# Performance work log

Hardware: AMD Instinct MI355X
Metric: run time of the kernel (lower is better)

## Reference

```python
import jax, jax.numpy as jnp
import numpy as np

D = 768
H = 12
HD = D // H
EPS = 1e-5

def layer_norm(x, g, b):
    xf = x.astype(jnp.float32)
    mu = jnp.mean(xf, axis=-1, keepdims=True)
    var = jnp.var(xf, axis=-1, keepdims=True)
    return ((xf - mu) * jax.lax.rsqrt(var + EPS) * g + b).astype(x.dtype)

def quick_gelu(x):
    return x * jax.nn.sigmoid(1.702 * x)

def setup_inputs() -> dict:
    key = jax.random.key(0)
    ks = jax.random.split(key, 8)
    L, N = 257, 64
    s = 1.0 / np.sqrt(D)
    return {
        "x": jax.random.normal(ks[0], (L, N, D), dtype=jnp.float32),
        "in_proj_w": jax.random.normal(ks[1], (3 * D, D), dtype=jnp.float32) * s,
        "in_proj_b": jnp.zeros((3 * D,), dtype=jnp.float32),
        "out_proj_w": jax.random.normal(ks[2], (D, D), dtype=jnp.float32) * s,
        "out_proj_b": jnp.zeros((D,), dtype=jnp.float32),
        "ln1_g": jnp.ones((D,), dtype=jnp.float32),
        "ln1_b": jnp.zeros((D,), dtype=jnp.float32),
        "ln2_g": jnp.ones((D,), dtype=jnp.float32),
        "ln2_b": jnp.zeros((D,), dtype=jnp.float32),
        "fc_w": jax.random.normal(ks[3], (D, D), dtype=jnp.float32) * s,
        "fc_b": jnp.zeros((D,), dtype=jnp.float32),
    }

def reference(x, in_proj_w, in_proj_b, out_proj_w, out_proj_b,
              ln1_g, ln1_b, ln2_g, ln2_b, fc_w, fc_b):
    L, N, _ = x.shape
    h = layer_norm(x, ln1_g, ln1_b)                      # [L,N,D]
    qkv = h @ in_proj_w.T + in_proj_b                    # [L,N,3D]
    q, k, v = jnp.split(qkv, 3, axis=-1)
    q = q.reshape(L, N, H, HD)
    k = k.reshape(L, N, H, HD)
    v = v.reshape(L, N, H, HD)
    scale = 1.0 / np.sqrt(HD)
    scores = jnp.einsum('lnhd,mnhd->nhlm', q, k) * scale  # [N,H,L,L]
    weights = jax.nn.softmax(scores, axis=-1)             # per-head attn weights
    attn = jnp.einsum('nhlm,mnhd->lnhd', weights, v).reshape(L, N, D)
    attn_out = attn @ out_proj_w.T + out_proj_b
    x = x + attn_out
    h2 = layer_norm(x, ln2_g, ln2_b)
    x = x + quick_gelu(h2 @ fc_w.T + fc_b)
    return x, weights
```

## Files before the change

kernel.cpp:

```cpp
#include <hip/hip_runtime.h>
#include <cstdint>

#define D_MODEL 768
#define NHEAD 12
#define HDIM 64
#define LSEQ 257
#define NBATCH 64
#define MROWS (LSEQ*NBATCH)

typedef unsigned short u16;
typedef __attribute__((ext_vector_type(8))) short short8;
typedef __attribute__((ext_vector_type(4))) float floatx4;

__device__ __forceinline__ float b2f(u16 u){ return __uint_as_float(((unsigned)u)<<16); }
__device__ __forceinline__ u16 f2bf(float f){
  unsigned x = __float_as_uint(f);
  return (u16)((x + 0x7fffu + ((x>>16)&1u)) >> 16);
}

__device__ __forceinline__ void async16(const u16* g, u16* l) {
  __builtin_amdgcn_global_load_lds(
      (const __attribute__((address_space(1))) unsigned int*)g,
      (__attribute__((address_space(3))) unsigned int*)l, 16, 0, 0);
}

__global__ __launch_bounds__(256) void cvt_bf16(const float* __restrict__ in,
                                                u16* __restrict__ out, int n8)
{
  int i = blockIdx.x*256 + threadIdx.x;
  if (i >= n8) return;
  const float4* p = (const float4*)in + (size_t)i*2;
  float4 a = p[0], b = p[1];
  u16 t[8] = {f2bf(a.x),f2bf(a.y),f2bf(a.z),f2bf(a.w),
              f2bf(b.x),f2bf(b.y),f2bf(b.z),f2bf(b.w)};
  *(uint4*)(out + (size_t)i*8) = *(const uint4*)t;
}

template<typename TIN>
__global__ __launch_bounds__(256) void ln_kernel(const TIN* __restrict__ x,
    const float* __restrict__ g, const float* __restrict__ b,
    u16* __restrict__ out, int rows)
{
  int wv = threadIdx.x >> 6, lane = threadIdx.x & 63;
  int row = blockIdx.x*4 + wv;
  if (row >= rows) return;
  const TIN* xr = x + (size_t)row*D_MODEL;
  float v[12]; float s = 0.f, s2 = 0.f;
#pragma unroll
  for (int i=0;i<12;++i){
    float f;
    if constexpr (sizeof(TIN)==2) f = b2f(((const u16*)xr)[lane + i*64]);
    else                          f = ((const float*)xr)[lane + i*64];
    v[i]=f; s+=f; s2+=f*f;
  }
#pragma unroll
  for (int o=32;o>0;o>>=1){ s += __shfl_xor(s,o,64); s2 += __shfl_xor(s2,o,64); }
  float mu = s*(1.f/768.f);
  float var = fmaxf(s2*(1.f/768.f) - mu*mu, 0.f);
  float rs = rsqrtf(var + 1e-5f);
  u16* orow = out + (size_t)row*D_MODEL;
#pragma unroll
  for (int i=0;i<12;++i){
    int c = lane + i*64;
    orow[c] = f2bf((v[i]-mu)*rs*g[c] + b[c]);
  }
}

#define BM 128
#define BN 128
#define BK 32

template<int EPI>
__global__ __launch_bounds__(256,2) void gemm_bt(
    const u16* __restrict__ A, const u16* __restrict__ B,
    const float* __restrict__ bias, void* __restrict__ Cout,
    const void* __restrict__ resid, int M, int N, int K)
{
  __shared__ u16 sA[BM*BK];
  __shared__ u16 sB[BN*BK];
  const int m0 = blockIdx.y * BM, n0 = blockIdx.x * BN;
  const int tid = threadIdx.x;
  const int lane = tid & 63, w = tid >> 6;
  const int wm = (w>>1)*64, wn = (w&1)*64;
  const int l16 = lane & 15, quad = lane >> 4;
  const int srow = lane >> 2, scol = (lane & 3)*8;
  int ar0 = m0 + w*32 + srow;      if (ar0 >= M) ar0 = M-1;
  int ar1 = m0 + w*32 + 16 + srow; if (ar1 >= M) ar1 = M-1;
  const u16* gA0 = A + (size_t)ar0*K + scol;
  const u16* gA1 = A + (size_t)ar1*K + scol;
  const u16* gB  = B + (size_t)(n0 + w*32 + srow)*K + scol;
  u16* lA0 = sA + w*32*BK;
  u16* lB0 = sB + w*32*BK;

  floatx4 acc[4][4];
#pragma unroll
  for (int i=0;i<4;++i)
#pragma unroll
    for (int j=0;j<4;++j) acc[i][j] = (floatx4){0.f,0.f,0.f,0.f};

  for (int k0=0;k0<K;k0+=BK) {
    async16(gA0 + k0,       lA0);
    async16(gA1 + k0,       lA0 + 16*BK);
    async16(gB  + k0,       lB0);
    async16(gB  + k0 + 16*K, lB0 + 16*BK);
    __syncthreads();
    short8 af[4], bfr[4];
#pragma unroll
    for (int t=0;t<4;++t) af[t]  = *(const short8*)(sA + (wm + t*16 + l16)*BK + quad*8);
#pragma unroll
    for (int t=0;t<4;++t) bfr[t] = *(const short8*)(sB + (wn + t*16 + l16)*BK + quad*8);
#pragma unroll
    for (int mt=0;mt<4;++mt)
#pragma unroll
      for (int nt=0;nt<4;++nt)
        acc[mt][nt] = __builtin_amdgcn_mfma_f32_16x16x32_bf16(af[mt], bfr[nt], acc[mt][nt], 0,0,0);
    __syncthreads();
  }

#pragma unroll
  for (int mt=0;mt<4;++mt)
#pragma unroll
    for (int nt=0;nt<4;++nt) {
      int col = n0 + wn + nt*16 + l16;
      if (col >= N) continue;
      float bia = bias[col];
      int rowb = m0 + wm + mt*16 + quad*4;
#pragma unroll
      for (int r=0;r<4;++r) {
        int row = rowb + r;
        if (row >= M) continue;
        float vacc = acc[mt][nt][r] + bia;
        size_t off = (size_t)row*N + col;
        if (EPI==0) {
          ((u16*)Cout)[off] = f2bf(vacc);
        } else if (EPI==1) {
          ((u16*)Cout)[off] = f2bf(((const float*)resid)[off] + vacc);
        } else {
          float gl = vacc / (1.f + __expf(-1.702f*vacc));
          ((float*)Cout)[off] = b2f(((const u16*)resid)[off]) + gl;
        }
      }
    }
}

__global__ __launch_bounds__(256,2) void attn_kernel(
    const u16* __restrict__ qkv, float* __restrict__ wout, u16* __restrict__ attn)
{
  __shared__ __align__(16) u16 smem[29696];
  u16* sQ  = smem;
  u16* sK  = smem + 64*72;
  u16* sP  = smem;
  u16* sVt = smem + 64*296;
  const int p = blockIdx.x;
  const int n = p / NHEAD, h = p % NHEAD;
  const int l0 = blockIdx.y * 64;
  const int tid = threadIdx.x, lane = tid & 63, w = tid >> 6;
  const int l16 = lane & 15, quad = lane >> 4;

  for (int i = tid; i < 64*8; i += 256) {
    int lr = i >> 3, c8 = (i & 7)*8;
    uint4 v = {0u,0u,0u,0u};
    int gl = l0 + lr;
    if (gl < LSEQ) v = *(const uint4*)(qkv + ((size_t)gl*NBATCH + n)*2304 + h*HDIM + c8);
    *(uint4*)(sQ + lr*72 + c8) = v;
  }
  for (int i = tid; i < 272*8; i += 256) {
    int kr = i >> 3, c8 = (i & 7)*8;
    uint4 v = {0u,0u,0u,0u};
    if (kr < LSEQ) v = *(const uint4*)(qkv + ((size_t)kr*NBATCH + n)*2304 + 768 + h*HDIM + c8);
    *(uint4*)(sK + kr*72 + c8) = v;
  }
  __syncthreads();

  floatx4 acc[17];
#pragma unroll
  for (int t=0;t<17;++t) acc[t] = (floatx4){0.f,0.f,0.f,0.f};
#pragma unroll
  for (int ks=0;ks<2;++ks) {
    short8 aq = *(const short8*)(sQ + (w*16 + l16)*72 + ks*32 + quad*8);
#pragma unroll
    for (int nt=0;nt<17;++nt) {
      short8 bk = *(const short8*)(sK + (nt*16 + l16)*72 + ks*32 + quad*8);
      acc[nt] = __builtin_amdgcn_mfma_f32_16x16x32_bf16(aq, bk, acc[nt], 0,0,0);
    }
  }
  __syncthreads();

#pragma unroll
  for (int r=0;r<4;++r) {
    float mx = -3.0e38f;
#pragma unroll
    for (int nt=0;nt<17;++nt) {
      int col = nt*16 + l16;
      float v = (col < LSEQ) ? acc[nt][r]*0.125f : -3.0e38f;
      acc[nt][r] = v;
      mx = fmaxf(mx, v);
    }
#pragma unroll
    for (int o=1;o<16;o<<=1) mx = fmaxf(mx, __shfl_xor(mx,o,64));
    float sum = 0.f;
#pragma unroll
    for (int nt=0;nt<17;++nt) {
      float e = __expf(acc[nt][r]-mx);
      acc[nt][r] = e; sum += e;
    }
#pragma unroll
    for (int o=1;o<16;o<<=1) sum += __shfl_xor(sum,o,64);
    float inv = 1.f/sum;
#pragma unroll
    for (int nt=0;nt<17;++nt) acc[nt][r] *= inv;
  }

  size_t wbase = (size_t)p * LSEQ * LSEQ;
#pragma unroll
  for (int r=0;r<4;++r) {
    int lr = w*16 + quad*4 + r;
    int gl = l0 + lr;
#pragma unroll
    for (int nt=0;nt<17;++nt) {
      int col = nt*16 + l16;
      sP[lr*296 + col] = f2bf(acc[nt][r]);
      if (gl < LSEQ && col < LSEQ) wout[wbase + (size_t)gl*LSEQ + col] = acc[nt][r];
    }
  }
  for (int i = tid; i < 64*16; i += 256) {
    int lr = i >> 4, c = 272 + (i & 15);
    sP[lr*296 + c] = 0;
  }
  __syncthreads();

  floatx4 acc2[4];
#pragma unroll
  for (int t=0;t<4;++t) acc2[t] = (floatx4){0.f,0.f,0.f,0.f};
  for (int c=0;c<2;++c) {
    if (c) __syncthreads();
    int mbase = c*160;
    int msz = c ? 128 : 160;
    for (int ml = tid; ml < msz; ml += 256) {
      int m = mbase + ml;
      if (m < LSEQ) {
        const u16* vr = qkv + ((size_t)m*NBATCH + n)*2304 + 1536 + h*HDIM;
#pragma unroll
        for (int d=0; d<64; ++d) sVt[d*168 + ml] = vr[d];
      } else {
#pragma unroll
        for (int d=0; d<64; ++d) sVt[d*168 + ml] = 0;
      }
    }
    __syncthreads();
    int nks = c ? 4 : 5;
    for (int ksl=0; ksl<nks; ++ksl) {
      short8 ap = *(const short8*)(sP + (w*16 + l16)*296 + mbase + ksl*32 + quad*8);
#pragma unroll
      for (int nt=0;nt<4;++nt) {
        short8 bv = *(const short8*)(sVt + (nt*16 + l16)*168 + ksl*32 + quad*8);
        acc2[nt] = __builtin_amdgcn_mfma_f32_16x16x32_bf16(ap, bv, acc2[nt], 0,0,0);
      }
    }
  }
#pragma unroll
  for (int nt=0;nt<4;++nt)
#pragma unroll
    for (int r=0;r<4;++r) {
      int lr = w*16 + quad*4 + r;
      int gl = l0 + lr;
      if (gl < LSEQ) {
        int d = nt*16 + l16;
        attn[((size_t)gl*NBATCH + n)*768 + h*HDIM + d] = f2bf(acc2[nt][r]);
      }
    }
}

extern "C" void kernel_launch(void* const* d_in, const int* in_sizes, int n_in,
                              void* d_out, int out_size, void* d_ws, size_t ws_size,
                              hipStream_t stream)
{
  (void)in_sizes; (void)n_in; (void)out_size; (void)ws_size;
  const float* x    = (const float*)d_in[0];
  const float* w_in = (const float*)d_in[1];
  const float* b_in = (const float*)d_in[2];
  const float* w_op = (const float*)d_in[3];
  const float* b_op = (const float*)d_in[4];
  const float* g1   = (const float*)d_in[5];
  const float* b1   = (const float*)d_in[6];
  const float* g2   = (const float*)d_in[7];
  const float* b2v  = (const float*)d_in[8];
  const float* wfc  = (const float*)d_in[9];
  const float* bfc  = (const float*)d_in[10];

  float* out_x = (float*)d_out;
  float* out_w = out_x + (size_t)MROWS*D_MODEL;

  char* ws = (char*)d_ws;
  u16* qkv  = (u16*)ws;
  u16* hbuf = (u16*)(ws + (size_t)MROWS*2304*2);
  u16* x2b  = (u16*)(ws + (size_t)MROWS*2304*2 + (size_t)MROWS*768*2);

  u16* w_in_bf = x2b;
  u16* w_op_bf = qkv + (size_t)24*1024*1024;
  u16* w_fc_bf = w_op_bf + 768*768;

  dim3 blk(256);
  cvt_bf16<<<dim3(864), blk, 0, stream>>>(w_in, w_in_bf, 221184);
  ln_kernel<float><<<dim3(MROWS/4), blk, 0, stream>>>(x, g1, b1, hbuf, MROWS);
  gemm_bt<0><<<dim3(18,129), blk, 0, stream>>>(hbuf, w_in_bf, b_in, qkv, nullptr, MROWS, 2304, 768);
  attn_kernel<<<dim3(768,5), blk, 0, stream>>>(qkv, out_w, hbuf);
  cvt_bf16<<<dim3(288), blk, 0, stream>>>(w_op, w_op_bf, 73728);
  cvt_bf16<<<dim3(288), blk, 0, stream>>>(wfc,  w_fc_bf, 73728);
  gemm_bt<1><<<dim3(6,129), blk, 0, stream>>>(hbuf, w_op_bf, b_op, x2b, x, MROWS, 768, 768);
  ln_kernel<u16><<<dim3(MROWS/4), blk, 0, stream>>>(x2b, g2, b2v, qkv, MROWS);
  gemm_bt<2><<<dim3(6,129), blk, 0, stream>>>(qkv, w_fc_bf, bfc, out_x, x2b, MROWS, 768, 768);
}
```

Before: 643.2 us.

## Pre-transpose V into a separate buffer so attention loads it with vector reads

Adds a kernel that transposes each head's V slice into a [head][d][m] layout through swizzled shared memory, and stores it in the not-yet-written output buffer. The attention kernel then fills its transposed-V tile with 16-byte vector loads instead of scalar strided global reads and scalar LDS writes. This removes uncoalesced V traffic that is repeated by all five query-tile blocks per head, at the cost of an extra launch and an extra global round trip of V.

```diff
diff --git a/kernel.cpp b/kernel.cpp
--- a/kernel.cpp
+++ b/kernel.cpp
@@ -7,6 +7,7 @@
 #define LSEQ 257
 #define NBATCH 64
 #define MROWS (LSEQ*NBATCH)
+#define VSTRIDE 288
 
 typedef unsigned short u16;
 typedef __attribute__((ext_vector_type(8))) short short8;
@@ -34,6 +35,37 @@
   u16 t[8] = {f2bf(a.x),f2bf(a.y),f2bf(a.z),f2bf(a.w),
               f2bf(b.x),f2bf(b.y),f2bf(b.z),f2bf(b.w)};
   *(uint4*)(out + (size_t)i*8) = *(const uint4*)t;
+}
+
+__global__ __launch_bounds__(256) void vtr_kernel(const u16* __restrict__ qkv,
+                                                  u16* __restrict__ vT)
+{
+  __shared__ __align__(16) u16 t[64][72];
+  const int p = blockIdx.x, mc = blockIdx.y;
+  const int n = p / NHEAD, h = p % NHEAD;
+  const int m0 = mc*64;
+  const int tid = threadIdx.x;
+  for (int i = tid; i < 512; i += 256) {
+    int mr = i >> 3, c8 = (i & 7)*8;
+    uint4 v = {0u,0u,0u,0u};
+    int m = m0 + mr;
+    if (m < LSEQ) v = *(const uint4*)(qkv + ((size_t)m*NBATCH + n)*2304 + 1536 + h*HDIM + c8);
+    *(uint4*)(&t[mr][c8 ^ ((mr&7)<<3)]) = v;
+  }
+  __syncthreads();
+  for (int i = tid; i < 512; i += 256) {
+    int d  = (i >> 1) & 63;
+    int mo = (((i & 1) | ((i >> 7) << 1))) * 8;
+    int mg = m0 + mo;
+    if (mg >= VSTRIDE) continue;
+    u16 tmp[8];
+#pragma unroll
+    for (int j = 0; j < 8; ++j) {
+      int mr = mo + j;
+      tmp[j] = t[mr][((d & ~7) ^ ((mr & 7) << 3)) | (d & 7)];
+    }
+    *(uint4*)(vT + ((size_t)p*HDIM + d)*VSTRIDE + mg) = *(const uint4*)tmp;
+  }
 }
 
 template<typename TIN>
@@ -99,9 +131,9 @@
     for (int j=0;j<4;++j) acc[i][j] = (floatx4){0.f,0.f,0.f,0.f};
 
   for (int k0=0;k0<K;k0+=BK) {
-    async16(gA0 + k0,       lA0);
-    async16(gA1 + k0,       lA0 + 16*BK);
-    async16(gB  + k0,       lB0);
+    async16(gA0 + k0,        lA0);
+    async16(gA1 + k0,        lA0 + 16*BK);
+    async16(gB  + k0,        lB0);
     async16(gB  + k0 + 16*K, lB0 + 16*BK);
     __syncthreads();
     short8 af[4], bfr[4];
@@ -144,7 +176,8 @@
 }
 
 __global__ __launch_bounds__(256,2) void attn_kernel(
-    const u16* __restrict__ qkv, float* __restrict__ wout, u16* __restrict__ attn)
+    const u16* __restrict__ qkv, const u16* __restrict__ vT,
+    float* __restrict__ wout, u16* __restrict__ attn)
 {
   __shared__ __align__(16) u16 smem[29696];
   u16* sQ  = smem;
@@ -229,6 +262,7 @@
   }
   __syncthreads();
 
+  const u16* vTp = vT + (size_t)p*HDIM*VSTRIDE;
   floatx4 acc2[4];
 #pragma unroll
   for (int t=0;t<4;++t) acc2[t] = (floatx4){0.f,0.f,0.f,0.f};
@@ -236,16 +270,11 @@
     if (c) __syncthreads();
     int mbase = c*160;
     int msz = c ? 128 : 160;
-    for (int ml = tid; ml < msz; ml += 256) {
-      int m = mbase + ml;
-      if (m < LSEQ) {
-        const u16* vr = qkv + ((size_t)m*NBATCH + n)*2304 + 1536 + h*HDIM;
-#pragma unroll
-        for (int d=0; d<64; ++d) sVt[d*168 + ml] = vr[d];
-      } else {
-#pragma unroll
-        for (int d=0; d<64; ++d) sVt[d*168 + ml] = 0;
-      }
+    int nvec = msz >> 3;
+    for (int i = tid; i < 64*nvec; i += 256) {
+      int d = i / nvec, jm = (i - d*nvec)*8;
+      uint4 v = *(const uint4*)(vTp + (size_t)d*VSTRIDE + mbase + jm);
+      *(uint4*)(sVt + d*168 + jm) = v;
     }
     __syncthreads();
     int nks = c ? 4 : 5;
@@ -299,12 +328,14 @@
   u16* w_in_bf = x2b;
   u16* w_op_bf = qkv + (size_t)24*1024*1024;
   u16* w_fc_bf = w_op_bf + 768*768;
+  u16* vT = (u16*)out_x;
 
   dim3 blk(256);
   cvt_bf16<<<dim3(864), blk, 0, stream>>>(w_in, w_in_bf, 221184);
   ln_kernel<float><<<dim3(MROWS/4), blk, 0, stream>>>(x, g1, b1, hbuf, MROWS);
   gemm_bt<0><<<dim3(18,129), blk, 0, stream>>>(hbuf, w_in_bf, b_in, qkv, nullptr, MROWS, 2304, 768);
-  attn_kernel<<<dim3(768,5), blk, 0, stream>>>(qkv, out_w, hbuf);
+  vtr_kernel<<<dim3(768,5), blk, 0, stream>>>(qkv, vT);
+  attn_kernel<<<dim3(768,5), blk, 0, stream>>>(qkv, vT, out_w, hbuf);
   cvt_bf16<<<dim3(288), blk, 0, stream>>>(w_op, w_op_bf, 73728);
   cvt_bf16<<<dim3(288), blk, 0, stream>>>(wfc,  w_fc_bf, 73728);
   gemm_bt<1><<<dim3(6,129), blk, 0, stream>>>(hbuf, w_op_bf, b_op, x2b, x, MROWS, 768, 768);
```

Measured after the change: 665.2 us. +3.4%, slower.

## Double-buffer GEMM LDS tiles with XOR swizzle and remap attention grid

Applied to the files above, without the earlier changes.

The GEMM now double-buffers its A/B LDS tiles. The next K-tile is prefetched with global_load_lds while the current tile is consumed, using explicit vmcnt waits and raw barriers. An XOR swizzle on the 16-byte column chunks is meant to reduce LDS bank conflicts on the fragment reads. The attention launch is flattened to a 1D grid with a remap that interleaves blocks across 8 groups, likely targeting XCD locality so blocks sharing K/V land on the same die. LDS use doubles, which may affect occupancy.

```diff
diff --git a/kernel.cpp b/kernel.cpp
--- a/kernel.cpp
+++ b/kernel.cpp
@@ -76,21 +76,22 @@
     const float* __restrict__ bias, void* __restrict__ Cout,
     const void* __restrict__ resid, int M, int N, int K)
 {
-  __shared__ u16 sA[BM*BK];
-  __shared__ u16 sB[BN*BK];
+  __shared__ u16 sA[2][BM*BK];
+  __shared__ u16 sB[2][BN*BK];
   const int m0 = blockIdx.y * BM, n0 = blockIdx.x * BN;
   const int tid = threadIdx.x;
   const int lane = tid & 63, w = tid >> 6;
   const int wm = (w>>1)*64, wn = (w&1)*64;
   const int l16 = lane & 15, quad = lane >> 4;
-  const int srow = lane >> 2, scol = (lane & 3)*8;
+  const int srow = lane >> 2;
+  const int scol = ((lane & 3) ^ ((srow >> 1) & 3)) * 8;
   int ar0 = m0 + w*32 + srow;      if (ar0 >= M) ar0 = M-1;
   int ar1 = m0 + w*32 + 16 + srow; if (ar1 >= M) ar1 = M-1;
   const u16* gA0 = A + (size_t)ar0*K + scol;
   const u16* gA1 = A + (size_t)ar1*K + scol;
-  const u16* gB  = B + (size_t)(n0 + w*32 + srow)*K + scol;
-  u16* lA0 = sA + w*32*BK;
-  u16* lB0 = sB + w*32*BK;
+  const u16* gB0 = B + (size_t)(n0 + w*32 + srow)*K + scol;
+  const u16* gB1 = B + (size_t)(n0 + w*32 + 16 + srow)*K + scol;
+  const int lw = w*32*BK;
 
   floatx4 acc[4][4];
 #pragma unroll
@@ -98,23 +99,40 @@
 #pragma unroll
     for (int j=0;j<4;++j) acc[i][j] = (floatx4){0.f,0.f,0.f,0.f};
 
-  for (int k0=0;k0<K;k0+=BK) {
-    async16(gA0 + k0,       lA0);
-    async16(gA1 + k0,       lA0 + 16*BK);
-    async16(gB  + k0,       lB0);
-    async16(gB  + k0 + 16*K, lB0 + 16*BK);
-    __syncthreads();
+  const int ntiles = K >> 5;
+  async16(gA0, &sA[0][lw]);
+  async16(gA1, &sA[0][lw + 16*BK]);
+  async16(gB0, &sB[0][lw]);
+  async16(gB1, &sB[0][lw + 16*BK]);
+
+  for (int t=0; t<ntiles; ++t) {
+    const int cur = t & 1;
+    if (t+1 < ntiles) {
+      const int k1 = (t+1)*BK;
+      async16(gA0 + k1, &sA[1-cur][lw]);
+      async16(gA1 + k1, &sA[1-cur][lw + 16*BK]);
+      async16(gB0 + k1, &sB[1-cur][lw]);
+      async16(gB1 + k1, &sB[1-cur][lw + 16*BK]);
+      asm volatile("s_waitcnt vmcnt(4)" ::: "memory");
+    } else {
+      asm volatile("s_waitcnt vmcnt(0)" ::: "memory");
+    }
+    __builtin_amdgcn_s_barrier();
+    __builtin_amdgcn_sched_barrier(0);
     short8 af[4], bfr[4];
 #pragma unroll
-    for (int t=0;t<4;++t) af[t]  = *(const short8*)(sA + (wm + t*16 + l16)*BK + quad*8);
-#pragma unroll
-    for (int t=0;t<4;++t) bfr[t] = *(const short8*)(sB + (wn + t*16 + l16)*BK + quad*8);
+    for (int tt=0;tt<4;++tt)
+      af[tt]  = *(const short8*)(&sA[cur][(wm + tt*16 + l16)*BK + (quad ^ ((l16>>1)&3))*8]);
+#pragma unroll
+    for (int tt=0;tt<4;++tt)
+      bfr[tt] = *(const short8*)(&sB[cur][(wn + tt*16 + l16)*BK + (quad ^ ((l16>>1)&3))*8]);
 #pragma unroll
     for (int mt=0;mt<4;++mt)
 #pragma unroll
       for (int nt=0;nt<4;++nt)
         acc[mt][nt] = __builtin_amdgcn_mfma_f32_16x16x32_bf16(af[mt], bfr[nt], acc[mt][nt], 0,0,0);
-    __syncthreads();
+    __builtin_amdgcn_sched_barrier(0);
+    __builtin_amdgcn_s_barrier();
   }
 
 #pragma unroll
@@ -151,9 +169,11 @@
   u16* sK  = smem + 64*72;
   u16* sP  = smem;
   u16* sVt = smem + 64*296;
-  const int p = blockIdx.x;
+  const int linear = blockIdx.x;
+  const int wi = (linear & 7)*480 + (linear >> 3);
+  const int p = wi / 5;
   const int n = p / NHEAD, h = p % NHEAD;
-  const int l0 = blockIdx.y * 64;
+  const int l0 = (wi % 5) * 64;
   const int tid = threadIdx.x, lane = tid & 63, w = tid >> 6;
   const int l16 = lane & 15, quad = lane >> 4;
 
@@ -304,7 +324,7 @@
   cvt_bf16<<<dim3(864), blk, 0, stream>>>(w_in, w_in_bf, 221184);
   ln_kernel<float><<<dim3(MROWS/4), blk, 0, stream>>>(x, g1, b1, hbuf, MROWS);
   gemm_bt<0><<<dim3(18,129), blk, 0, stream>>>(hbuf, w_in_bf, b_in, qkv, nullptr, MROWS, 2304, 768);
-  attn_kernel<<<dim3(768,5), blk, 0, stream>>>(qkv, out_w, hbuf);
+  attn_kernel<<<dim3(3840), blk, 0, stream>>>(qkv, out_w, hbuf);
   cvt_bf16<<<dim3(288), blk, 0, stream>>>(w_op, w_op_bf, 73728);
   cvt_bf16<<<dim3(288), blk, 0, stream>>>(wfc,  w_fc_bf, 73728);
   gemm_bt<1><<<dim3(6,129), blk, 0, stream>>>(hbuf, w_op_bf, b_op, x2b, x, MROWS, 768, 768);
```

Result: no change. 643.4 us (+0.0%).
